# Performance work log

Measured on AMD Instinct MI355X. Metric: run time of the kernel, lower is better.

## Reference

```python
import jax, jax.numpy as jnp
import numpy as np

N = 50000        # nodes
E = 800000       # edges (avg degree 16)
HID = 256        # hidden_size
HEADS = 8        # num_heads
HD = HID // HEADS  # head_dim = 32


def setup_inputs() -> dict:
    key = jax.random.key(0)
    ks = jax.random.split(key, 10)
    h = jax.random.normal(ks[0], (N, HID), dtype=jnp.float32)
    val = jax.random.uniform(ks[1], (E,), dtype=jnp.float32)
    Wq = jax.random.normal(ks[2], (HID, HID), dtype=jnp.float32) * 0.02
    Wk = jax.random.normal(ks[3], (HID, HID), dtype=jnp.float32) * 0.02
    Wv = jax.random.normal(ks[4], (HID, HID), dtype=jnp.float32) * 0.02
    bq = jnp.zeros((HID,), dtype=jnp.float32)
    bk = jnp.zeros((HID,), dtype=jnp.float32)
    bv = jnp.zeros((HID,), dtype=jnp.float32)
    # CSR rows expanded to per-edge row ids (sorted, like row_ptr expansion)
    edge_rows = jnp.sort(jax.random.randint(ks[5], (E,), 0, N, dtype=jnp.int32))
    col_ind = jax.random.randint(ks[6], (E,), 0, N, dtype=jnp.int32)
    return {"h": h, "val": val, "Wq": Wq, "bq": bq, "Wk": Wk, "bk": bk,
            "Wv": Wv, "bv": bv, "edge_rows": edge_rows, "col_ind": col_ind}


def reference(h, val, Wq, bq, Wk, bk, Wv, bv, edge_rows, col_ind):
    scaling = HD ** (-0.5)
    # projections; reshape splits hidden as (head_dim, heads) with heads fastest,
    # exactly as in the torch module: reshape(N, head_dim, num_heads)
    q = ((h @ Wq + bq).reshape(N, HD, HEADS)) * scaling
    k = (h @ Wk + bk).reshape(N, HD, HEADS)
    v = (h @ Wv + bv).reshape(N, HD, HEADS)

    # SDDMM restricted to edges: score[e, head] = <q[row_e], k[col_e]> * A.val[e]
    score = jnp.einsum('edh,edh->eh', q[edge_rows], k[col_ind]) * val[:, None]  # [E, HEADS]

    # per-destination-row softmax over incident edges (stable, segment ops)
    m = jax.ops.segment_max(score, edge_rows, num_segments=N)        # [N, HEADS]
    m = jnp.where(jnp.isfinite(m), m, jnp.zeros_like(m))             # empty rows
    e = jnp.exp(score - m[edge_rows])                                # [E, HEADS]
    denom = jax.ops.segment_sum(e, edge_rows, num_segments=N)        # [N, HEADS]
    attn = e / denom[edge_rows]

    # SpMM: out[i] = sum over edges (i, j) of attn * v[j]
    contrib = attn[:, None, :] * v[col_ind]                          # [E, HD, HEADS]
    out = jax.ops.segment_sum(contrib, edge_rows, num_segments=N)    # [N, HD, HEADS]
    return out.reshape(N, -1)                                        # [N, HID]
```

## Files before the change

### kernel.cpp

```cpp
#include <hip/hip_runtime.h>
#include <hip/hip_bf16.h>
#include <math.h>

static constexpr int kN   = 50000;
static constexpr int kE   = 800000;
static constexpr int kHID = 256;
static constexpr int kHD  = 32;

typedef short bf16x8 __attribute__((ext_vector_type(8)));
typedef float f32x4  __attribute__((ext_vector_type(4)));
typedef float f32x2  __attribute__((ext_vector_type(2)));
typedef unsigned short us8 __attribute__((ext_vector_type(8)));
typedef unsigned int u32x4 __attribute__((ext_vector_type(4)));
typedef int i32x2 __attribute__((ext_vector_type(2)));
typedef int i32x4 __attribute__((ext_vector_type(4)));

__device__ __forceinline__ float b2f(unsigned short u) {
  union { unsigned v; float f; } c; c.v = ((unsigned)u) << 16; return c.f;
}

__device__ __forceinline__ unsigned short f2bu(float f) {
  __hip_bfloat16 b = __float2bfloat16(f);
  union { __hip_bfloat16 b; unsigned short u; } c; c.b = b; return c.u;
}

__device__ __forceinline__ f32x2 bf2up(unsigned u) {
  union { unsigned v; float f; } lo, hi;
  lo.v = u << 16; hi.v = u & 0xffff0000u;
  return f32x2{lo.f, hi.f};
}

__device__ __forceinline__ float quad_add_xor1(float s) {
  union { float f; int i; } a, b;
  a.f = s;
  b.i = __builtin_amdgcn_mov_dpp(a.i, 0xB1, 0xF, 0xF, true);
  return s + b.f;
}
__device__ __forceinline__ float quad_add_xor2(float s) {
  union { float f; int i; } a, b;
  a.f = s;
  b.i = __builtin_amdgcn_mov_dpp(a.i, 0x4E, 0xF, 0xF, true);
  return s + b.f;
}

__device__ __forceinline__ void load_lds16(const void* g, void* l) {
  __builtin_amdgcn_global_load_lds(
      (const __attribute__((address_space(1))) unsigned int*)(unsigned long long)(uintptr_t)g,
      (__attribute__((address_space(3))) unsigned int*)(unsigned int)(uintptr_t)l,
      16, 0, 0);
}

__global__ void split_h_kernel(const float* __restrict__ h,
                               __hip_bfloat16* __restrict__ Ah) {
  int idx = blockIdx.x * 256 + threadIdx.x;
  const f32x4* hp = (const f32x4*)(h + (size_t)idx * 8);
  f32x4 a = hp[0], b = hp[1];
  us8 o;
  o[0] = f2bu(a[0]); o[1] = f2bu(a[1]); o[2] = f2bu(a[2]); o[3] = f2bu(a[3]);
  o[4] = f2bu(b[0]); o[5] = f2bu(b[1]); o[6] = f2bu(b[2]); o[7] = f2bu(b[3]);
  *(us8*)(Ah + (size_t)idx * 8) = o;
}

__global__ void build_bt_kernel(const float* __restrict__ Wq, const float* __restrict__ bq,
                                const float* __restrict__ Wk, const float* __restrict__ bk,
                                const float* __restrict__ Wv, const float* __restrict__ bv,
                                __hip_bfloat16* __restrict__ Bt, float* __restrict__ biasP) {
  const int n  = blockIdx.x;
  const int kk = threadIdx.x;
  const int g  = n >> 8;
  const int cc = n & 255;
  const int c  = ((cc & 31) << 3) + (cc >> 5);
  const float scale = (g == 0) ? 0.17677669529663689f : 1.0f;
  const float* W = (g == 0) ? Wq : ((g == 1) ? Wk : Wv);
  Bt[n * 256 + kk] = __float2bfloat16(W[kk * 256 + c] * scale);
  if (kk == 0) {
    const float* b = (g == 0) ? bq : ((g == 1) ? bk : bv);
    biasP[n] = b[c] * scale;
  }
}

__global__ void prep_kernel(const int* __restrict__ er, int* __restrict__ rp,
                            const int* __restrict__ ci, const float* __restrict__ vl,
                            i32x2* __restrict__ cv) {
  const int b = blockIdx.x;
  if (b < 196) {
    int i = b * 256 + threadIdx.x;
    if (i > kN) return;
    int lo = 0, hi = kE;
    while (lo < hi) {
      int mid = (lo + hi) >> 1;
      if (er[mid] < i) lo = mid + 1; else hi = mid;
    }
    rp[i] = lo;
  } else {
    const int e4 = ((b - 196) * 256 + threadIdx.x) * 4;
    if (e4 < kE) {
      i32x4 c = *(const i32x4*)(ci + e4);
      f32x4 w = *(const f32x4*)(vl + e4);
      i32x4 o0 = {c[0], __float_as_int(w[0]), c[1], __float_as_int(w[1])};
      i32x4 o1 = {c[2], __float_as_int(w[2]), c[3], __float_as_int(w[3])};
      *(i32x4*)(cv + e4)     = o0;
      *(i32x4*)(cv + e4 + 2) = o1;
    }
  }
}

__global__ __launch_bounds__(256) void gemm_qkv_kernel(
    const __hip_bfloat16* __restrict__ Ah,
    const __hip_bfloat16* __restrict__ Bt, const float* __restrict__ biasP,
    __hip_bfloat16* __restrict__ qb, __hip_bfloat16* __restrict__ kvb) {
  __shared__ __align__(16) char smemRaw[34816];
  short* smemA = (short*)smemRaw;
  short* smemB = (short*)(smemRaw + 16384);
  short* smemC = (short*)smemRaw;

  const int L   = blockIdx.x;
  const int xcd = L & 7;
  const int t   = L >> 3;
  const int nt  = t % 6;
  const int mg  = t / 6;
  const int mt  = mg * 8 + xcd;
  if (mt >= 391) return;
  const int colBase = nt * 128;
  const int rowBase = mt * 128;

  const int tid  = threadIdx.x;
  const int wave = tid >> 6;
  const int lane = tid & 63;
  const int wm = wave & 1;
  const int wn = wave >> 1;

  f32x4 acc[4][4];
#pragma unroll
  for (int i = 0; i < 4; ++i)
#pragma unroll
    for (int j = 0; j < 4; ++j) acc[i][j] = f32x4{0.f, 0.f, 0.f, 0.f};

  for (int k0 = 0; k0 < 256; k0 += 64) {
    __syncthreads();
#pragma unroll
    for (int j = 0; j < 4; ++j) {
      int s = (wave * 4 + j) * 64 + lane;
      int r = s >> 3, cp = s & 7;
      int c = cp ^ (r & 7);
      int grow = rowBase + r;
      grow = grow < kN ? grow : kN - 1;
      const char* gp = (const char*)Ah + (size_t)grow * 512 + k0 * 2 + c * 16;
      load_lds16(gp, (char*)smemA + (wave * 4 + j) * 1024);
    }
#pragma unroll
    for (int j = 0; j < 4; ++j) {
      int s = (wave * 4 + j) * 64 + lane;
      int r = s >> 3, cp = s & 7;
      int c = cp ^ (r & 7);
      const char* gp = (const char*)Bt + (size_t)(colBase + r) * 512 + k0 * 2 + c * 16;
      load_lds16(gp, (char*)smemB + (wave * 4 + j) * 1024);
    }
    __syncthreads();

    const int rq = lane & 15, qd = lane >> 4;
#pragma unroll
    for (int ks = 0; ks < 2; ++ks) {
      bf16x8 af[4], bfr[4];
#pragma unroll
      for (int mi = 0; mi < 4; ++mi) {
        int r = wm * 64 + mi * 16 + rq;
        int c = (ks * 4 + qd) ^ (r & 7);
        af[mi] = *(const bf16x8*)&smemA[r * 64 + c * 8];
      }
#pragma unroll
      for (int nj = 0; nj < 4; ++nj) {
        int r = wn * 64 + nj * 16 + rq;
        int c = (ks * 4 + qd) ^ (r & 7);
        bfr[nj] = *(const bf16x8*)&smemB[r * 64 + c * 8];
      }
#pragma unroll
      for (int mi = 0; mi < 4; ++mi)
#pragma unroll
        for (int nj = 0; nj < 4; ++nj)
          acc[mi][nj] = __builtin_amdgcn_mfma_f32_16x16x32_bf16(
              af[mi], bfr[nj], acc[mi][nj], 0, 0, 0);
    }
  }

  __syncthreads();
#pragma unroll
  for (int nj = 0; nj < 4; ++nj) {
    const int cl = wn * 64 + nj * 16 + (lane & 15);
    const float bb = biasP[colBase + cl];
#pragma unroll
    for (int mi = 0; mi < 4; ++mi) {
      const int rl = wm * 64 + mi * 16 + (lane >> 4) * 4;
#pragma unroll
      for (int reg = 0; reg < 4; ++reg) {
        smemC[(rl + reg) * 136 + cl] = (short)f2bu(acc[mi][nj][reg] + bb);
      }
    }
  }
  __syncthreads();

  const int g = colBase >> 8;
#pragma unroll
  for (int it = 0; it < 8; ++it) {
    const int r   = it * 16 + (tid >> 4);
    const int c16 = tid & 15;
    const int row = rowBase + r;
    if (row < kN) {
      bf16x8 vls = *(const bf16x8*)&smemC[r * 136 + c16 * 8];
      const int cc = (colBase & 255) + c16 * 8;
      __hip_bfloat16* dst =
          (g == 0) ? (qb + (size_t)row * 256 + cc)
                   : (kvb + (size_t)row * 512 + (g == 2 ? 256 : 0) + cc);
      *(bf16x8*)dst = vls;
    }
  }
}

__global__ __launch_bounds__(128) void edge_attn_kernel(
    const __hip_bfloat16* __restrict__ qb, const __hip_bfloat16* __restrict__ kvb,
    const int* __restrict__ row_ptr, const i32x2* __restrict__ cvp,
    float* __restrict__ out) {
  const int wave = threadIdx.x >> 6;
  const int lane = threadIdx.x & 63;
  const int half = lane >> 5;
  const int sl   = lane & 31;
  const int row = blockIdx.x * 2 + wave;
  if (row >= kN) return;

  const int e0 = row_ptr[row];
  const int e1 = row_ptr[row + 1];

  const us8 qu = *(const us8*)(qb + (size_t)row * 256 + sl * 8);
  f32x2 qf2[4];
#pragma unroll
  for (int j = 0; j < 4; ++j)
    qf2[j] = f32x2{b2f(qu[2 * j]) * 1.4426950408889634f,
                   b2f(qu[2 * j + 1]) * 1.4426950408889634f};

  float denom = 0.f;
  f32x2 acc2[4];
#pragma unroll
  for (int j = 0; j < 4; ++j) acc2[j] = f32x2{0.f, 0.f};

  if (e0 < e1) {
    const char* kvbL = (const char*)kvb + sl * 16;
    const int elast = e1 - 1;

    u32x4 kS[4], vS[4];
    float wS[4];
    i32x2 cvA[4], cvB[4];

    i32x2 c0[4];
#pragma unroll
    for (int j = 0; j < 4; ++j) {
      const int ea = min(e0 + 2 * j + half, elast);
      c0[j] = cvp[ea];
    }
#pragma unroll
    for (int j = 0; j < 4; ++j) {
      const int eb = min(e0 + 8 + 2 * j + half, elast);
      cvA[j] = cvp[eb];
    }
#pragma unroll
    for (int j = 0; j < 4; ++j) {
      const int ec = min(e0 + 16 + 2 * j + half, elast);
      cvB[j] = cvp[ec];
    }
#pragma unroll
    for (int j = 0; j < 4; ++j) {
      const size_t off = (size_t)c0[j][0] * 1024;
      kS[j] = *(const u32x4*)(kvbL + off);
      vS[j] = *(const u32x4*)(kvbL + off + 512);
      wS[j] = __int_as_float(c0[j][1]);
    }

#define ATTN_GROUP(EB, CB)                                                \
    _Pragma("unroll")                                                     \
    for (int j = 0; j < 4; ++j) {                                         \
      const u32x4 kc = kS[j], vc = vS[j];                                 \
      const float wc = wS[j];                                             \
      {                                                                   \
        const size_t off = (size_t)CB[j][0] * 1024;                       \
        kS[j] = *(const u32x4*)(kvbL + off);                              \
        vS[j] = *(const u32x4*)(kvbL + off + 512);                        \
        wS[j] = __int_as_float(CB[j][1]);                                 \
      }                                                                   \
      {                                                                   \
        const int en = min((EB) + 24 + 2 * j + half, elast);              \
        CB[j] = cvp[en];                                                  \
      }                                                                   \
      f32x2 s2 = qf2[0] * bf2up(kc[0]);                                   \
      s2 += qf2[1] * bf2up(kc[1]);                                        \
      s2 += qf2[2] * bf2up(kc[2]);                                        \
      s2 += qf2[3] * bf2up(kc[3]);                                        \
      float s = s2[0] + s2[1];                                            \
      s = quad_add_xor1(s);                                               \
      s = quad_add_xor2(s);                \
      s *= wc;                                                            \
      float p = exp2f(s);                                                 \
      p = (((EB) + 2 * j + half) < e1) ? p : 0.f;                         \
      denom += p;                                                         \
      const f32x2 p2 = {p, p};                                            \
      acc2[0] += p2 * bf2up(vc[0]);                                       \
      acc2[1] += p2 * bf2up(vc[1]);                                       \
      acc2[2] += p2 * bf2up(vc[2]);                                       \
      acc2[3] += p2 * bf2up(vc[3]);                                       \
    }

    int e = e0;
    for (;;) {
      ATTN_GROUP(e, cvA);
      e += 8; if (e >= e1) break;
      ATTN_GROUP(e, cvB);
      e += 8; if (e >= e1) break;
    }
#undef ATTN_GROUP
  }

  float accs[8];
#pragma unroll
  for (int j = 0; j < 8; ++j) {
    float a = (j & 1) ? acc2[j >> 1][1] : acc2[j >> 1][0];
    accs[j] = a + __shfl_xor(a, 32);
  }
  denom += __shfl_xor(denom, 32);

  const float inv = (denom > 0.f) ? (1.0f / denom) : 0.f;
  const int h = sl >> 2;
  const int dbase = (sl & 3) * 8 + half * 4;
  float* o = out + (size_t)row * 256 + h;
#pragma unroll
  for (int jj = 0; jj < 4; ++jj)
    o[(dbase + jj) * 8] = accs[half * 4 + jj] * inv;
}

extern "C" void kernel_launch(void* const* d_in, const int* in_sizes, int n_in,
                              void* d_out, int out_size, void* d_ws, size_t ws_size,
                              hipStream_t stream) {
  const float* h   = (const float*)d_in[0];
  const float* val = (const float*)d_in[1];
  const float* Wq  = (const float*)d_in[2];
  const float* bq  = (const float*)d_in[3];
  const float* Wk  = (const float*)d_in[4];
  const float* bk  = (const float*)d_in[5];
  const float* Wv  = (const float*)d_in[6];
  const float* bv  = (const float*)d_in[7];
  const int* edge_rows = (const int*)d_in[8];
  const int* col_ind   = (const int*)d_in[9];
  float* out = (float*)d_out;

  char* ws = (char*)d_ws;
  __hip_bfloat16* Ah  = (__hip_bfloat16*)ws;                 ws += (size_t)kN * 256 * 2;
  __hip_bfloat16* Bt  = (__hip_bfloat16*)ws;                 ws += (size_t)768 * 256 * 2;
  float*          biasP = (float*)ws;                        ws += 768 * 4;
  __hip_bfloat16* qb  = (__hip_bfloat16*)ws;                 ws += (size_t)kN * 256 * 2;
  __hip_bfloat16* kvb = (__hip_bfloat16*)ws;                 ws += (size_t)kN * 512 * 2;
  int* row_ptr = (int*)ws;                                   ws += ((size_t)(kN + 1) * 4 + 127) & ~127ull;
  i32x2* cv = (i32x2*)ws;

  split_h_kernel<<<kN / 8, 256, 0, stream>>>(h, Ah);
  build_bt_kernel<<<768, 256, 0, stream>>>(Wq, bq, Wk, bk, Wv, bv, Bt, biasP);
  prep_kernel<<<196 + 782, 256, 0, stream>>>(edge_rows, row_ptr, col_ind, val, cv);

  gemm_qkv_kernel<<<8 * 6 * 49, 256, 0, stream>>>(Ah, Bt, biasP, qb, kvb);

  edge_attn_kernel<<<(kN + 1) / 2, 128, 0, stream>>>(qb, kvb, row_ptr, cv, out);
}
```

Measured before the change: 270.3 us.

## Merge prep kernels into one launch and double the edge-gather prefetch depth

Folds the three preprocessing kernels (h to bf16, the weight transpose/scale, and row_ptr plus col/val packing) into a single kernel that dispatches on block index, removing two launches and their gaps. The edge attention kernel now keeps two sets of prefetched K/V registers, so gathers for the next two 8-edge groups are in flight rather than one. The aim is to hide more gather latency, at the cost of more VGPRs and possibly lower occupancy.

```diff
diff --git a/kernel.cpp b/kernel.cpp
--- a/kernel.cpp
+++ b/kernel.cpp
@@ -50,39 +50,43 @@
       16, 0, 0);
 }
 
-__global__ void split_h_kernel(const float* __restrict__ h,
-                               __hip_bfloat16* __restrict__ Ah) {
-  int idx = blockIdx.x * 256 + threadIdx.x;
-  const f32x4* hp = (const f32x4*)(h + (size_t)idx * 8);
-  f32x4 a = hp[0], b = hp[1];
-  us8 o;
-  o[0] = f2bu(a[0]); o[1] = f2bu(a[1]); o[2] = f2bu(a[2]); o[3] = f2bu(a[3]);
-  o[4] = f2bu(b[0]); o[5] = f2bu(b[1]); o[6] = f2bu(b[2]); o[7] = f2bu(b[3]);
-  *(us8*)(Ah + (size_t)idx * 8) = o;
-}
-
-__global__ void build_bt_kernel(const float* __restrict__ Wq, const float* __restrict__ bq,
-                                const float* __restrict__ Wk, const float* __restrict__ bk,
-                                const float* __restrict__ Wv, const float* __restrict__ bv,
-                                __hip_bfloat16* __restrict__ Bt, float* __restrict__ biasP) {
-  const int n  = blockIdx.x;
-  const int kk = threadIdx.x;
-  const int g  = n >> 8;
-  const int cc = n & 255;
-  const int c  = ((cc & 31) << 3) + (cc >> 5);
-  const float scale = (g == 0) ? 0.17677669529663689f : 1.0f;
-  const float* W = (g == 0) ? Wq : ((g == 1) ? Wk : Wv);
-  Bt[n * 256 + kk] = __float2bfloat16(W[kk * 256 + c] * scale);
-  if (kk == 0) {
-    const float* b = (g == 0) ? bq : ((g == 1) ? bk : bv);
-    biasP[n] = b[c] * scale;
-  }
-}
-
-__global__ void prep_kernel(const int* __restrict__ er, int* __restrict__ rp,
-                            const int* __restrict__ ci, const float* __restrict__ vl,
-                            i32x2* __restrict__ cv) {
-  const int b = blockIdx.x;
+__global__ void prep_all_kernel(
+    const float* __restrict__ h, __hip_bfloat16* __restrict__ Ah,
+    const float* __restrict__ Wq, const float* __restrict__ bq,
+    const float* __restrict__ Wk, const float* __restrict__ bk,
+    const float* __restrict__ Wv, const float* __restrict__ bv,
+    __hip_bfloat16* __restrict__ Bt, float* __restrict__ biasP,
+    const int* __restrict__ er, int* __restrict__ rp,
+    const int* __restrict__ ci, const float* __restrict__ vl,
+    i32x2* __restrict__ cv) {
+  int b = blockIdx.x;
+  if (b < 6250) {
+    int idx = b * 256 + threadIdx.x;
+    const f32x4* hp = (const f32x4*)(h + (size_t)idx * 8);
+    f32x4 a = hp[0], c = hp[1];
+    us8 o;
+    o[0] = f2bu(a[0]); o[1] = f2bu(a[1]); o[2] = f2bu(a[2]); o[3] = f2bu(a[3]);
+    o[4] = f2bu(c[0]); o[5] = f2bu(c[1]); o[6] = f2bu(c[2]); o[7] = f2bu(c[3]);
+    *(us8*)(Ah + (size_t)idx * 8) = o;
+    return;
+  }
+  b -= 6250;
+  if (b < 768) {
+    const int n  = b;
+    const int kk = threadIdx.x;
+    const int g  = n >> 8;
+    const int cc = n & 255;
+    const int c  = ((cc & 31) << 3) + (cc >> 5);
+    const float scale = (g == 0) ? 0.17677669529663689f : 1.0f;
+    const float* W = (g == 0) ? Wq : ((g == 1) ? Wk : Wv);
+    Bt[n * 256 + kk] = __float2bfloat16(W[kk * 256 + c] * scale);
+    if (kk == 0) {
+      const float* bb = (g == 0) ? bq : ((g == 1) ? bk : bv);
+      biasP[n] = bb[c] * scale;
+    }
+    return;
+  }
+  b -= 768;
   if (b < 196) {
     int i = b * 256 + threadIdx.x;
     if (i > kN) return;
@@ -92,8 +96,11 @@
       if (er[mid] < i) lo = mid + 1; else hi = mid;
     }
     rp[i] = lo;
-  } else {
-    const int e4 = ((b - 196) * 256 + threadIdx.x) * 4;
+    return;
+  }
+  b -= 196;
+  {
+    const int e4 = (b * 256 + threadIdx.x) * 4;
     if (e4 < kE) {
       i32x4 c = *(const i32x4*)(ci + e4);
       f32x4 w = *(const f32x4*)(vl + e4);
@@ -246,48 +253,48 @@
     const char* kvbL = (const char*)kvb + sl * 16;
     const int elast = e1 - 1;
 
-    u32x4 kS[4], vS[4];
-    float wS[4];
+    u32x4 kSa[4], vSa[4], kSb[4], vSb[4];
+    float wSa[4], wSb[4];
     i32x2 cvA[4], cvB[4];
 
-    i32x2 c0[4];
+    i32x2 c00[4], c01[4];
+#pragma unroll
+    for (int j = 0; j < 4; ++j) c00[j] = cvp[min(e0 +      2 * j + half, elast)];
+#pragma unroll
+    for (int j = 0; j < 4; ++j) c01[j] = cvp[min(e0 +  8 + 2 * j + half, elast)];
+#pragma unroll
+    for (int j = 0; j < 4; ++j) cvA[j] = cvp[min(e0 + 16 + 2 * j + half, elast)];
+#pragma unroll
+    for (int j = 0; j < 4; ++j) cvB[j] = cvp[min(e0 + 24 + 2 * j + half, elast)];
 #pragma unroll
     for (int j = 0; j < 4; ++j) {
-      const int ea = min(e0 + 2 * j + half, elast);
-      c0[j] = cvp[ea];
+      const size_t off = (size_t)c00[j][0] * 1024;
+      kSa[j] = *(const u32x4*)(kvbL + off);
+      vSa[j] = *(const u32x4*)(kvbL + off + 512);
+      wSa[j] = __int_as_float(c00[j][1]);
     }
 #pragma unroll
     for (int j = 0; j < 4; ++j) {
-      const int eb = min(e0 + 8 + 2 * j + half, elast);
-      cvA[j] = cvp[eb];
-    }
-#pragma unroll
-    for (int j = 0; j < 4; ++j) {
-      const int ec = min(e0 + 16 + 2 * j + half, elast);
-      cvB[j] = cvp[ec];
-    }
-#pragma unroll
-    for (int j = 0; j < 4; ++j) {
-      const size_t off = (size_t)c0[j][0] * 1024;
-      kS[j] = *(const u32x4*)(kvbL + off);
-      vS[j] = *(const u32x4*)(kvbL + off + 512);
-      wS[j] = __int_as_float(c0[j][1]);
-    }
-
-#define ATTN_GROUP(EB, CB)                                                \
+      const size_t off = (size_t)c01[j][0] * 1024;
+      kSb[j] = *(const u32x4*)(kvbL + off);
+      vSb[j] = *(const u32x4*)(kvbL + off + 512);
+      wSb[j] = __int_as_float(c01[j][1]);
+    }
+
+#define ATTN_GROUP(EB, KS, VS, WS, CV)                                    \
     _Pragma("unroll")                                                     \
     for (int j = 0; j < 4; ++j) {                                         \
-      const u32x4 kc = kS[j], vc = vS[j];                                 \
-      const float wc = wS[j];                                             \
+      const u32x4 kc = KS[j], vc = VS[j];                                 \
+      const float wc = WS[j];                                             \
       {                                                                   \
-        const size_t off = (size_t)CB[j][0] * 1024;                       \
-        kS[j] = *(const u32x4*)(kvbL + off);                              \
-        vS[j] = *(const u32x4*)(kvbL + off + 512);                        \
-        wS[j] = __int_as_float(CB[j][1]);                                 \
+        const size_t off = (size_t)CV[j][0] * 1024;                       \
+        KS[j] = *(const u32x4*)(kvbL + off);                              \
+        VS[j] = *(const u32x4*)(kvbL + off + 512);                        \
+        WS[j] = __int_as_float(CV[j][1]);                                 \
       }                                                                   \
       {                                                                   \
-        const int en = min((EB) + 24 + 2 * j + half, elast);              \
-        CB[j] = cvp[en];                                                  \
+        const int en = min((EB) + 32 + 2 * j + half, elast);              \
+        CV[j] = cvp[en];                                                  \
       }                                                                   \
       f32x2 s2 = qf2[0] * bf2up(kc[0]);                                   \
       s2 += qf2[1] * bf2up(kc[1]);                                        \
@@ -309,9 +316,9 @@
 
     int e = e0;
     for (;;) {
-      ATTN_GROUP(e, cvA);
+      ATTN_GROUP(e, kSa, vSa, wSa, cvA);
       e += 8; if (e >= e1) break;
-      ATTN_GROUP(e, cvB);
+      ATTN_GROUP(e, kSb, vSb, wSb, cvB);
       e += 8; if (e >= e1) break;
     }
 #undef ATTN_GROUP
@@ -358,9 +365,9 @@
   int* row_ptr = (int*)ws;                                   ws += ((size_t)(kN + 1) * 4 + 127) & ~127ull;
   i32x2* cv = (i32x2*)ws;
 
-  split_h_kernel<<<kN / 8, 256, 0, stream>>>(h, Ah);
-  build_bt_kernel<<<768, 256, 0, stream>>>(Wq, bq, Wk, bk, Wv, bv, Bt, biasP);
-  prep_kernel<<<196 + 782, 256, 0, stream>>>(edge_rows, row_ptr, col_ind, val, cv);
+  prep_all_kernel<<<6250 + 768 + 196 + 782, 256, 0, stream>>>(
+      h, Ah, Wq, bq, Wk, bk, Wv, bv, Bt, biasP,
+      edge_rows, row_ptr, col_ind, val, cv);
 
   gemm_qkv_kernel<<<8 * 6 * 49, 256, 0, stream>>>(Ah, Bt, biasP, qb, kvb);
 
```

Result: no change. 269.5 us (-0.3%).

## Merge preprocessing kernels into one launch and double-buffer GEMM LDS stages

Applied to the files above, without the earlier changes.

The three small preprocessing kernels (h to bf16 conversion, weight transpose and bias packing, row_ptr and edge packing) are merged into one launch that dispatches by block index range. This removes two launch gaps. The QKV GEMM now double-buffers its LDS tiles in 64 KB of shared memory, issuing the next k-slice's global-to-LDS loads before computing on the current one, with one barrier per iteration. The larger LDS footprint may lower the number of blocks resident per CU.

```diff
diff --git a/kernel.cpp b/kernel.cpp
--- a/kernel.cpp
+++ b/kernel.cpp
@@ -50,39 +50,43 @@
       16, 0, 0);
 }
 
-__global__ void split_h_kernel(const float* __restrict__ h,
-                               __hip_bfloat16* __restrict__ Ah) {
-  int idx = blockIdx.x * 256 + threadIdx.x;
-  const f32x4* hp = (const f32x4*)(h + (size_t)idx * 8);
-  f32x4 a = hp[0], b = hp[1];
-  us8 o;
-  o[0] = f2bu(a[0]); o[1] = f2bu(a[1]); o[2] = f2bu(a[2]); o[3] = f2bu(a[3]);
-  o[4] = f2bu(b[0]); o[5] = f2bu(b[1]); o[6] = f2bu(b[2]); o[7] = f2bu(b[3]);
-  *(us8*)(Ah + (size_t)idx * 8) = o;
-}
-
-__global__ void build_bt_kernel(const float* __restrict__ Wq, const float* __restrict__ bq,
-                                const float* __restrict__ Wk, const float* __restrict__ bk,
-                                const float* __restrict__ Wv, const float* __restrict__ bv,
-                                __hip_bfloat16* __restrict__ Bt, float* __restrict__ biasP) {
-  const int n  = blockIdx.x;
-  const int kk = threadIdx.x;
-  const int g  = n >> 8;
-  const int cc = n & 255;
-  const int c  = ((cc & 31) << 3) + (cc >> 5);
-  const float scale = (g == 0) ? 0.17677669529663689f : 1.0f;
-  const float* W = (g == 0) ? Wq : ((g == 1) ? Wk : Wv);
-  Bt[n * 256 + kk] = __float2bfloat16(W[kk * 256 + c] * scale);
-  if (kk == 0) {
-    const float* b = (g == 0) ? bq : ((g == 1) ? bk : bv);
-    biasP[n] = b[c] * scale;
-  }
-}
-
-__global__ void prep_kernel(const int* __restrict__ er, int* __restrict__ rp,
-                            const int* __restrict__ ci, const float* __restrict__ vl,
-                            i32x2* __restrict__ cv) {
-  const int b = blockIdx.x;
+__global__ void prep_all_kernel(
+    const float* __restrict__ h, __hip_bfloat16* __restrict__ Ah,
+    const float* __restrict__ Wq, const float* __restrict__ bq,
+    const float* __restrict__ Wk, const float* __restrict__ bk,
+    const float* __restrict__ Wv, const float* __restrict__ bv,
+    __hip_bfloat16* __restrict__ Bt, float* __restrict__ biasP,
+    const int* __restrict__ er, int* __restrict__ rp,
+    const int* __restrict__ ci, const float* __restrict__ vl,
+    i32x2* __restrict__ cv) {
+  int b = blockIdx.x;
+  if (b < 6250) {
+    int idx = b * 256 + threadIdx.x;
+    const f32x4* hp = (const f32x4*)(h + (size_t)idx * 8);
+    f32x4 a = hp[0], c = hp[1];
+    us8 o;
+    o[0] = f2bu(a[0]); o[1] = f2bu(a[1]); o[2] = f2bu(a[2]); o[3] = f2bu(a[3]);
+    o[4] = f2bu(c[0]); o[5] = f2bu(c[1]); o[6] = f2bu(c[2]); o[7] = f2bu(c[3]);
+    *(us8*)(Ah + (size_t)idx * 8) = o;
+    return;
+  }
+  b -= 6250;
+  if (b < 768) {
+    const int n  = b;
+    const int kk = threadIdx.x;
+    const int g  = n >> 8;
+    const int cc = n & 255;
+    const int c  = ((cc & 31) << 3) + (cc >> 5);
+    const float scale = (g == 0) ? 0.17677669529663689f : 1.0f;
+    const float* W = (g == 0) ? Wq : ((g == 1) ? Wk : Wv);
+    Bt[n * 256 + kk] = __float2bfloat16(W[kk * 256 + c] * scale);
+    if (kk == 0) {
+      const float* bb = (g == 0) ? bq : ((g == 1) ? bk : bv);
+      biasP[n] = bb[c] * scale;
+    }
+    return;
+  }
+  b -= 768;
   if (b < 196) {
     int i = b * 256 + threadIdx.x;
     if (i > kN) return;
@@ -92,8 +96,11 @@
       if (er[mid] < i) lo = mid + 1; else hi = mid;
     }
     rp[i] = lo;
-  } else {
-    const int e4 = ((b - 196) * 256 + threadIdx.x) * 4;
+    return;
+  }
+  b -= 196;
+  {
+    const int e4 = (b * 256 + threadIdx.x) * 4;
     if (e4 < kE) {
       i32x4 c = *(const i32x4*)(ci + e4);
       f32x4 w = *(const f32x4*)(vl + e4);
@@ -109,16 +116,14 @@
     const __hip_bfloat16* __restrict__ Ah,
     const __hip_bfloat16* __restrict__ Bt, const float* __restrict__ biasP,
     __hip_bfloat16* __restrict__ qb, __hip_bfloat16* __restrict__ kvb) {
-  __shared__ __align__(16) char smemRaw[34816];
-  short* smemA = (short*)smemRaw;
-  short* smemB = (short*)(smemRaw + 16384);
+  __shared__ __align__(16) char smemRaw[65536];
   short* smemC = (short*)smemRaw;
 
   const int L   = blockIdx.x;
   const int xcd = L & 7;
-  const int t   = L >> 3;
-  const int nt  = t % 6;
-  const int mg  = t / 6;
+  const int t_  = L >> 3;
+  const int nt  = t_ % 6;
+  const int mg  = t_ / 6;
   const int mt  = mg * 8 + xcd;
   if (mt >= 391) return;
   const int colBase = nt * 128;
@@ -136,29 +141,33 @@
 #pragma unroll
     for (int j = 0; j < 4; ++j) acc[i][j] = f32x4{0.f, 0.f, 0.f, 0.f};
 
-  for (int k0 = 0; k0 < 256; k0 += 64) {
-    __syncthreads();
-#pragma unroll
-    for (int j = 0; j < 4; ++j) {
-      int s = (wave * 4 + j) * 64 + lane;
-      int r = s >> 3, cp = s & 7;
-      int c = cp ^ (r & 7);
-      int grow = rowBase + r;
-      grow = grow < kN ? grow : kN - 1;
-      const char* gp = (const char*)Ah + (size_t)grow * 512 + k0 * 2 + c * 16;
-      load_lds16(gp, (char*)smemA + (wave * 4 + j) * 1024);
-    }
-#pragma unroll
-    for (int j = 0; j < 4; ++j) {
-      int s = (wave * 4 + j) * 64 + lane;
-      int r = s >> 3, cp = s & 7;
-      int c = cp ^ (r & 7);
-      const char* gp = (const char*)Bt + (size_t)(colBase + r) * 512 + k0 * 2 + c * 16;
-      load_lds16(gp, (char*)smemB + (wave * 4 + j) * 1024);
-    }
-    __syncthreads();
-
-    const int rq = lane & 15, qd = lane >> 4;
+#define STAGE(BUF, K0)                                                      \
+  {                                                                         \
+    char* dA = smemRaw + (BUF) * 32768;                                     \
+    char* dB = dA + 16384;                                                  \
+    _Pragma("unroll")                                                       \
+    for (int j = 0; j < 4; ++j) {                                           \
+      int s = (wave * 4 + j) * 64 + lane;                                   \
+      int r = s >> 3, cp = s & 7;                                           \
+      int c = cp ^ (r & 7);                                                 \
+      int grow = rowBase + r;                                               \
+      grow = grow < kN ? grow : kN - 1;                                     \
+      load_lds16((const char*)Ah + (size_t)grow * 512 + (K0) * 2 + c * 16,  \
+                 dA + (wave * 4 + j) * 1024);                               \
+      load_lds16((const char*)Bt + (size_t)(colBase + r) * 512 + (K0) * 2 + c * 16, \
+                 dB + (wave * 4 + j) * 1024);                               \
+    }                                                                       \
+  }
+
+  STAGE(0, 0);
+  __syncthreads();
+
+  const int rq = lane & 15, qd = lane >> 4;
+#pragma unroll
+  for (int t = 0; t < 4; ++t) {
+    if (t < 3) STAGE((t + 1) & 1, (t + 1) * 64);
+    const short* sA = (const short*)(smemRaw + (t & 1) * 32768);
+    const short* sB = sA + 8192;
 #pragma unroll
     for (int ks = 0; ks < 2; ++ks) {
       bf16x8 af[4], bfr[4];
@@ -166,13 +175,13 @@
       for (int mi = 0; mi < 4; ++mi) {
         int r = wm * 64 + mi * 16 + rq;
         int c = (ks * 4 + qd) ^ (r & 7);
-        af[mi] = *(const bf16x8*)&smemA[r * 64 + c * 8];
+        af[mi] = *(const bf16x8*)&sA[r * 64 + c * 8];
       }
 #pragma unroll
       for (int nj = 0; nj < 4; ++nj) {
         int r = wn * 64 + nj * 16 + rq;
         int c = (ks * 4 + qd) ^ (r & 7);
-        bfr[nj] = *(const bf16x8*)&smemB[r * 64 + c * 8];
+        bfr[nj] = *(const bf16x8*)&sB[r * 64 + c * 8];
       }
 #pragma unroll
       for (int mi = 0; mi < 4; ++mi)
@@ -181,9 +190,10 @@
           acc[mi][nj] = __builtin_amdgcn_mfma_f32_16x16x32_bf16(
               af[mi], bfr[nj], acc[mi][nj], 0, 0, 0);
     }
-  }
-
-  __syncthreads();
+    __syncthreads();
+  }
+#undef STAGE
+
 #pragma unroll
   for (int nj = 0; nj < 4; ++nj) {
     const int cl = wn * 64 + nj * 16 + (lane & 15);
@@ -358,9 +368,9 @@
   int* row_ptr = (int*)ws;                                   ws += ((size_t)(kN + 1) * 4 + 127) & ~127ull;
   i32x2* cv = (i32x2*)ws;
 
-  split_h_kernel<<<kN / 8, 256, 0, stream>>>(h, Ah);
-  build_bt_kernel<<<768, 256, 0, stream>>>(Wq, bq, Wk, bk, Wv, bv, Bt, biasP);
-  prep_kernel<<<196 + 782, 256, 0, stream>>>(edge_rows, row_ptr, col_ind, val, cv);
+  prep_all_kernel<<<6250 + 768 + 196 + 782, 256, 0, stream>>>(
+      h, Ah, Wq, bq, Wk, bk, Wv, bv, Bt, biasP,
+      edge_rows, row_ptr, col_ind, val, cv);
 
   gemm_qkv_kernel<<<8 * 6 * 49, 256, 0, stream>>>(Ah, Bt, biasP, qb, kvb);
 
```

Result: no change. 265.7 us, median of 2 (-1.7%).
